# Kernel tuning notes

Hardware: AMD Instinct MI355X
Metric: run time of the kernel (lower is better)

The kernel has to match this reference:

```python
import jax, jax.numpy as jnp
import numpy as np

N = 4096
FEAT = 5
H = 128
L = 3
K = 4
HD = H // K  # 32


def setup_inputs() -> dict:
    key = jax.random.key(0)
    ks = jax.random.split(key, 24)
    node_features = jax.random.normal(ks[0], (N, FEAT), dtype=jnp.float32)
    u = jax.random.uniform(ks[1], (N, N), dtype=jnp.float32)
    adj = jnp.where(u < 0.01, u, 0.0)
    adj = adj / (adj.sum(axis=1, keepdims=True) + 1e-8)  # row-normalised
    mask = jax.random.randint(ks[2], (N,), 0, 2).astype(bool)
    s = 0.05
    return {
        'node_features': node_features,
        'adj': adj,
        'mask': mask,
        'Wi': jax.random.normal(ks[3], (FEAT, H), jnp.float32) * s,
        'bi': jnp.zeros((H,), jnp.float32),
        'gat_W': jax.random.normal(ks[4], (L, K, H, HD), jnp.float32) * s,
        'gat_a': jax.random.normal(ks[5], (L, K, 2 * HD), jnp.float32) * s,
        'ln_g': jnp.ones((L, H), jnp.float32),
        'ln_b': jnp.zeros((L, H), jnp.float32),
        'pW1': jax.random.normal(ks[6], (H, H // 2), jnp.float32) * s,
        'pb1': jnp.zeros((H // 2,), jnp.float32),
        'pW2': jax.random.normal(ks[7], (H // 2, 1), jnp.float32) * s,
        'pb2': jnp.zeros((1,), jnp.float32),
        'poolW': jax.random.normal(ks[8], (H, H), jnp.float32) * s,
        'poolb': jnp.zeros((H,), jnp.float32),
        'poolv': jax.random.normal(ks[9], (H,), jnp.float32) * s,
        'vW1': jax.random.normal(ks[10], (H, H // 2), jnp.float32) * s,
        'vb1': jnp.zeros((H // 2,), jnp.float32),
        'vW2': jax.random.normal(ks[11], (H // 2, 1), jnp.float32) * s,
        'vb2': jnp.zeros((1,), jnp.float32),
    }


def _layernorm(x, g, b, eps=1e-5):
    mu = x.mean(-1, keepdims=True)
    var = ((x - mu) ** 2).mean(-1, keepdims=True)
    return (x - mu) / jnp.sqrt(var + eps) * g + b


def reference(node_features, adj, mask, Wi, bi, gat_W, gat_a, ln_g, ln_b,
              pW1, pb1, pW2, pb2, poolW, poolb, poolv, vW1, vb1, vW2, vb2):
    n = node_features.shape[0]
    x = jax.nn.relu(node_features @ Wi + bi)  # (N, H)
    edge_mask = (adj > 0) | jnp.eye(n, dtype=bool)  # (N, N) incl self-loops
    n_layers = gat_W.shape[0]
    for l in range(n_layers):
        Wx = jnp.einsum('nd,kdh->knh', x, gat_W[l])  # (K, N, hd)
        a_src = jnp.einsum('knh,kh->kn', Wx, gat_a[l][:, :HD])  # (K, N)
        a_dst = jnp.einsum('knh,kh->kn', Wx, gat_a[l][:, HD:])  # (K, N)
        e = jax.nn.leaky_relu(a_src[:, :, None] + a_dst[:, None, :], 0.2)  # (K,N,N)
        e = jnp.where(edge_mask[None], e, -jnp.inf)
        alpha = jax.nn.softmax(e, axis=-1)  # softmax over neighbours j
        h = jax.nn.elu(jnp.einsum('kij,kjh->kih', alpha, Wx))  # (K, N, hd)
        out = jnp.transpose(h, (1, 0, 2)).reshape(n, -1)  # concat heads -> (N, H)
        out = out + x  # residual (Identity: in_dim == out_dim)
        x = _layernorm(out, ln_g[l], ln_b[l])
    # policy head
    logits = (jax.nn.relu(x @ pW1 + pb1) @ pW2 + pb2).squeeze(-1)  # (N,)
    logits = jnp.where(mask, logits, -jnp.inf)
    # attention pooling restricted to masked (valid) nodes
    scores = jnp.tanh(x @ poolW + poolb) @ poolv  # (N,)
    scores = jnp.where(mask, scores, -jnp.inf)
    beta = jax.nn.softmax(scores)
    pooled = (beta[:, None] * x).sum(0)  # (H,)
    value = (jax.nn.relu(pooled @ vW1 + vb1) @ vW2 + vb2).squeeze(-1)  # scalar
    return logits, value
```

## Files before the change

kernel.cpp:

```cpp
#include <hip/hip_runtime.h>

#define NN 4096
#define FEAT 5
#define H 128
#define HD 32
#define KH 4
#define NEG_INF (-__builtin_inff())
#define MASK_SENTINEL (-1e30f)

#define WS_FLAG  0
#define WS_DEG   256
#define WS_NBR   (WS_DEG + NN*4)
#define WS_X     (WS_NBR + NN*128*2)
#define WS_WX    (WS_X + NN*H*4)
#define WS_ATS   (WS_WX + KH*NN*HD*4)
#define WS_ATD   (WS_ATS + NN*16)
#define WS_PART  (WS_ATD + NN*16)
#define WS_ZPART (WS_PART + 256*H*4)

__device__ __forceinline__ float red64(float v) {
#pragma unroll
    for (int off = 32; off; off >>= 1) v += __shfl_xor(v, off, 64);
    return v;
}
__device__ __forceinline__ float red32(float v) {
#pragma unroll
    for (int off = 16; off; off >>= 1) v += __shfl_xor(v, off, 32);
    return v;
}
__device__ __forceinline__ float red32max(float v) {
#pragma unroll
    for (int off = 16; off; off >>= 1) v = fmaxf(v, __shfl_xor(v, off, 32));
    return v;
}
__device__ __forceinline__ bool read_mask(const void* mp, int f, int n) {
    if (f == 3) return ((const long long*)mp)[n] != 0;
    if (f == 1) return ((const int*)mp)[n] != 0;
    if (f == 2) return ((const float*)mp)[n] != 0.f;
    return ((const unsigned char*)mp)[n] != 0;
}

__global__ __launch_bounds__(256) void k_proj(
    const float* __restrict__ nf, const float* __restrict__ Wi,
    const float* __restrict__ bi, const void* mask, int* flag,
    float* __restrict__ xbuf) {
    int w = threadIdx.x >> 6, lane = threadIdx.x & 63;
    int n = blockIdx.x * 4 + w;
    float a1 = bi[lane], a2 = bi[64 + lane];
#pragma unroll
    for (int f = 0; f < FEAT; f++) {
        float xv = nf[n * FEAT + f];
        a1 += xv * Wi[f * H + lane];
        a2 += xv * Wi[f * H + 64 + lane];
    }
    xbuf[(size_t)n * H + lane] = fmaxf(a1, 0.f);
    xbuf[(size_t)n * H + 64 + lane] = fmaxf(a2, 0.f);
    if (blockIdx.x == 0 && w == 0) {
        const unsigned* ip = (const unsigned*)mask;
        const float* fp = (const float*)mask;
        bool i32ok = true, i64ok = true, f32ok = true;
        for (int i = lane; i < 1024; i += 64) {
            unsigned v = ip[i];
            if (v > 1u) i32ok = false;
            if (i & 1) { if (v != 0u) i64ok = false; }
            else       { if (v > 1u) i64ok = false; }
            float fv = fp[i];
            if (fv != 0.f && fv != 1.f) f32ok = false;
        }
        i32ok = (__ballot((int)i32ok) == ~0ull);
        i64ok = (__ballot((int)i64ok) == ~0ull);
        f32ok = (__ballot((int)f32ok) == ~0ull);
        if (lane == 0) *flag = i64ok ? 3 : (i32ok ? 1 : (f32ok ? 2 : 0));
    }
}

__global__ __launch_bounds__(256) void k_csr(
    const float* __restrict__ adj, int* __restrict__ deg,
    unsigned short* __restrict__ nbr) {
    __shared__ int ln[4][128];
    int w = threadIdx.x >> 6, lane = threadIdx.x & 63;
    int row = blockIdx.x * 4 + w;
    ln[w][lane] = 0; ln[w][64 + lane] = 0;
    const float4* arow = (const float4*)(adj + (size_t)row * NN);
    int cnt = 0;
    bool self = false;
    for (int c0 = 0; c0 < NN / 4; c0 += 64) {
        float4 v = arow[c0 + lane];
        int cb = (c0 + lane) * 4;
        float vals[4] = {v.x, v.y, v.z, v.w};
#pragma unroll
        for (int s = 0; s < 4; s++) {
            bool nz = vals[s] > 0.f;
            if (nz && cb + s == row) self = true;
            unsigned long long b = __ballot((int)nz);
            if (nz) {
                int pos = cnt + __popcll(b & ((1ull << lane) - 1ull));
                if (pos < 128) ln[w][pos] = cb + s;
            }
            cnt += __popcll(b);
        }
    }
    bool anyself = __any((int)self);
    if (!anyself) {
        if (lane == 0 && cnt < 128) ln[w][cnt] = row;
        cnt++;
    }
    int d = cnt < 128 ? cnt : 128;
    if (lane == 0) deg[row] = d;
    nbr[(size_t)row * 128 + lane] = (unsigned short)ln[w][lane];
    nbr[(size_t)row * 128 + 64 + lane] = (unsigned short)ln[w][64 + lane];
}

__global__ __launch_bounds__(256) void k_wx(
    const float* __restrict__ xbuf, const float* __restrict__ gw,
    const float* __restrict__ ga, float* __restrict__ Wx,
    float* __restrict__ attS, float* __restrict__ attD) {
    __shared__ float xs[8][H];
    int t = threadIdx.x;
    int k = t >> 6, lane = t & 63, dh = lane >> 5, h = lane & 31;
    int n0 = blockIdx.x * 8;
    ((float4*)xs)[t] = ((const float4*)(xbuf + (size_t)n0 * H))[t];
    __syncthreads();
    float acc[8] = {0, 0, 0, 0, 0, 0, 0, 0};
    const float* g = gw + (size_t)k * (H * HD) + h;
    for (int dd = 0; dd < 64; dd += 4) {
        int d = dh * 64 + dd;
        float w0 = g[(size_t)(d + 0) * HD];
        float w1 = g[(size_t)(d + 1) * HD];
        float w2 = g[(size_t)(d + 2) * HD];
        float w3 = g[(size_t)(d + 3) * HD];
#pragma unroll
        for (int nn = 0; nn < 8; nn++) {
            float4 xv = *(const float4*)&xs[nn][d];
            acc[nn] += xv.x * w0 + xv.y * w1 + xv.z * w2 + xv.w * w3;
        }
    }
    float aws = ga[k * 64 + h], awd = ga[k * 64 + 32 + h];
#pragma unroll
    for (int nn = 0; nn < 8; nn++) {
        float full = acc[nn] + __shfl_xor(acc[nn], 32, 64);
        float s = red32(full * aws);
        float dv = red32(full * awd);
        int n = n0 + nn;
        if (dh == 0) Wx[(size_t)k * NN * HD + (size_t)n * HD + h] = full;
        if (lane == 0) { attS[n * 4 + k] = s; attD[n * 4 + k] = dv; }
    }
}

__global__ __launch_bounds__(256) void k_agg(
    const int* __restrict__ degG, const unsigned short* __restrict__ nbrG,
    const float* __restrict__ Wx, const float4* __restrict__ attS4,
    const float4* __restrict__ attD4, const float* __restrict__ lng,
    const float* __restrict__ lnb, float* __restrict__ xbuf) {
    __shared__ int lds_nbr[4][128];
    __shared__ float lds_al[4][2][128];
    __shared__ float lds_red[2][2][2];
    int t = threadIdx.x, w = t >> 6, lane = t & 63;
    int nn = w >> 1, wp = w & 1;
    int node = blockIdx.x * 2 + nn;
    int hs = lane >> 5, h = lane & 31;
    int k = 2 * wp + hs;
    int d = degG[node];
    {
        const unsigned short* np = nbrG + (size_t)node * 128;
        ushort2 a = *(const ushort2*)(np + lane * 2);
        lds_nbr[w][lane * 2] = a.x;
        lds_nbr[w][lane * 2 + 1] = a.y;
    }
    float4 aSv = attS4[node];
    float ai = wp ? (hs ? aSv.w : aSv.z) : (hs ? aSv.y : aSv.x);
    float e[4];
#pragma unroll
    for (int r = 0; r < 4; r++) {
        int c = r * 32 + h;
        if (c < d) {
            float4 dv4 = attD4[lds_nbr[w][c]];
            float dvv = wp ? (hs ? dv4.w : dv4.z) : (hs ? dv4.y : dv4.x);
            float v = ai + dvv;
            e[r] = v > 0.f ? v : 0.2f * v;
        } else e[r] = NEG_INF;
    }
    float m = red32max(fmaxf(fmaxf(e[0], e[1]), fmaxf(e[2], e[3])));
    float p[4], s = 0.f;
#pragma unroll
    for (int r = 0; r < 4; r++) {
        p[r] = (r * 32 + h < d) ? __expf(e[r] - m) : 0.f;
        s += p[r];
    }
    s = red32(s);
    float inv = 1.f / s;
#pragma unroll
    for (int r = 0; r < 4; r++) lds_al[w][hs][r * 32 + h] = p[r] * inv;
    float acc = 0.f;
    const float* wxk = Wx + (size_t)k * NN * HD + h;
    const float* ap = lds_al[w][hs];
    const int* np2 = lds_nbr[w];
    int dpad = (d + 7) & ~7;
    for (int c0 = 0; c0 < dpad; c0 += 8) {
        float a0 = ap[c0], a1 = ap[c0+1], a2 = ap[c0+2], a3 = ap[c0+3];
        float a4 = ap[c0+4], a5 = ap[c0+5], a6 = ap[c0+6], a7 = ap[c0+7];
        int s0 = np2[c0], s1 = np2[c0+1], s2 = np2[c0+2], s3 = np2[c0+3];
        int s4 = np2[c0+4], s5 = np2[c0+5], s6 = np2[c0+6], s7 = np2[c0+7];
        float v0 = wxk[(size_t)s0 * HD], v1 = wxk[(size_t)s1 * HD];
        float v2 = wxk[(size_t)s2 * HD], v3 = wxk[(size_t)s3 * HD];
        float v4 = wxk[(size_t)s4 * HD], v5 = wxk[(size_t)s5 * HD];
        float v6 = wxk[(size_t)s6 * HD], v7 = wxk[(size_t)s7 * HD];
        acc += a0*v0 + a1*v1 + a2*v2 + a3*v3 + a4*v4 + a5*v5 + a6*v6 + a7*v7;
    }
    float hv = acc > 0.f ? acc : __expf(acc) - 1.f;
    int dim = wp * 64 + lane;
    float o = hv + xbuf[(size_t)node * H + dim];
    float ps = red64(o);
    if (lane == 0) lds_red[nn][wp][0] = ps;
    __syncthreads();
    float mu = (lds_red[nn][0][0] + lds_red[nn][1][0]) * (1.f / H);
    float dv = o - mu;
    float vs = red64(dv * dv);
    if (lane == 0) lds_red[nn][wp][1] = vs;
    __syncthreads();
    float var = (lds_red[nn][0][1] + lds_red[nn][1][1]) * (1.f / H);
    float rstd = rsqrtf(var + 1e-5f);
    xbuf[(size_t)node * H + dim] = dv * rstd * lng[dim] + lnb[dim];
}

__global__ __launch_bounds__(256) void k_heads(
    const float* __restrict__ xbuf, const float* __restrict__ pW1,
    const float* __restrict__ pb1, const float* __restrict__ pW2,
    const float* __restrict__ pb2, const float* __restrict__ poolW,
    const float* __restrict__ poolb, const float* __restrict__ poolv,
    const void* mask, const int* __restrict__ flag, float* __restrict__ out,
    float* __restrict__ part, float* __restrict__ zpart) {
    __shared__ float lds_x[16][H];
    __shared__ float lds_part[4][H];
    __shared__ float lds_z[4];
    int t = threadIdx.x, w = t >> 6, lane = t & 63;
    int n0b = blockIdx.x * 16;
    for (int idx = t; idx < 16 * H; idx += 256)
        lds_x[idx >> 7][idx & 127] = xbuf[(size_t)(n0b + (idx >> 7)) * H + (idx & 127)];
    __syncthreads();
    int nb = n0b + w * 4;
    float accp[4] = {0, 0, 0, 0}, acs1[4] = {0, 0, 0, 0}, acs2[4] = {0, 0, 0, 0};
#pragma unroll 2
    for (int d = 0; d < H; d++) {
        float w1 = pW1[d * 64 + lane];
        float q1 = poolW[d * H + lane];
        float q2 = poolW[d * H + 64 + lane];
#pragma unroll
        for (int nn = 0; nn < 4; nn++) {
            float xv = lds_x[w * 4 + nn][d];
            accp[nn] += xv * w1;
            acs1[nn] += xv * q1;
            acs2[nn] += xv * q2;
        }
    }
    int flg = *flag;
    float T = fminf(red64(fabsf(poolv[lane]) + fabsf(poolv[64 + lane])), 30.f);
    float pb1v = pb1[lane], pw2v = pW2[lane], pb2v = pb2[0];
    float pob1 = poolb[lane], pob2 = poolb[64 + lane];
    float pov1 = poolv[lane], pov2 = poolv[64 + lane];
    float pp1 = 0.f, pp2 = 0.f, zacc = 0.f;
#pragma unroll
    for (int nn = 0; nn < 4; nn++) {
        int node = nb + nn;
        float hp = red64(fmaxf(accp[nn] + pb1v, 0.f) * pw2v);
        float sc = red64(tanhf(acs1[nn] + pob1) * pov1 + tanhf(acs2[nn] + pob2) * pov2);
        bool mk = read_mask(mask, flg, node);
        if (lane == 0) out[node] = mk ? (hp + pb2v) : MASK_SENTINEL;
        float wn = mk ? __expf(sc - T) : 0.f;
        pp1 += wn * lds_x[w * 4 + nn][lane];
        pp2 += wn * lds_x[w * 4 + nn][64 + lane];
        zacc += wn;
    }
    lds_part[w][lane] = pp1;
    lds_part[w][64 + lane] = pp2;
    if (lane == 0) lds_z[w] = zacc;
    __syncthreads();
    if (w == 0) {
        float s1 = lds_part[0][lane] + lds_part[1][lane] + lds_part[2][lane] + lds_part[3][lane];
        float s2 = lds_part[0][64 + lane] + lds_part[1][64 + lane] +
                   lds_part[2][64 + lane] + lds_part[3][64 + lane];
        part[blockIdx.x * H + lane] = s1;
        part[blockIdx.x * H + 64 + lane] = s2;
        if (lane == 0) zpart[blockIdx.x] = lds_z[0] + lds_z[1] + lds_z[2] + lds_z[3];
    }
}

__global__ __launch_bounds__(256) void k_value(
    const float* __restrict__ part, const float* __restrict__ zpart,
    const float* __restrict__ vW1, const float* __restrict__ vb1,
    const float* __restrict__ vW2, const float* __restrict__ vb2,
    float* __restrict__ out) {
    __shared__ float fin[2][H];
    __shared__ float zfin[256];
    __shared__ float pooled[H];
    int t = threadIdx.x;
    int dim = t & 127, hb = t >> 7;
    float s = 0.f;
    for (int b = hb * 128; b < hb * 128 + 128; b++) s += part[b * H + dim];
    fin[hb][dim] = s;
    zfin[t] = zpart[t];
    __syncthreads();
    for (int off = 128; off; off >>= 1) {
        if (t < off) zfin[t] += zfin[t + off];
        __syncthreads();
    }
    float Z = zfin[0];
    if (t < H) pooled[t] = (fin[0][t] + fin[1][t]) / Z;
    __syncthreads();
    if (t < 64) {
        float acc = vb1[t];
        for (int d = 0; d < H; d++) acc += pooled[d] * vW1[d * 64 + t];
        float v = red64(fmaxf(acc, 0.f) * vW2[t]);
        if (t == 0) out[NN] = v + vb2[0];
    }
}

extern "C" void kernel_launch(void* const* d_in, const int* in_sizes, int n_in,
                              void* d_out, int out_size, void* d_ws, size_t ws_size,
                              hipStream_t stream) {
    const float* nf    = (const float*)d_in[0];
    const float* adj   = (const float*)d_in[1];
    const void*  mask  = d_in[2];
    const float* Wi    = (const float*)d_in[3];
    const float* bi    = (const float*)d_in[4];
    const float* gat_W = (const float*)d_in[5];
    const float* gat_a = (const float*)d_in[6];
    const float* ln_g  = (const float*)d_in[7];
    const float* ln_b  = (const float*)d_in[8];
    const float* pW1   = (const float*)d_in[9];
    const float* pb1   = (const float*)d_in[10];
    const float* pW2   = (const float*)d_in[11];
    const float* pb2   = (const float*)d_in[12];
    const float* poolW = (const float*)d_in[13];
    const float* poolb = (const float*)d_in[14];
    const float* poolv = (const float*)d_in[15];
    const float* vW1   = (const float*)d_in[16];
    const float* vb1   = (const float*)d_in[17];
    const float* vW2   = (const float*)d_in[18];
    const float* vb2   = (const float*)d_in[19];

    char* ws = (char*)d_ws;
    int*            flag = (int*)(ws + WS_FLAG);
    int*            deg  = (int*)(ws + WS_DEG);
    unsigned short* nbr  = (unsigned short*)(ws + WS_NBR);
    float* xbuf  = (float*)(ws + WS_X);
    float* Wx    = (float*)(ws + WS_WX);
    float* ats   = (float*)(ws + WS_ATS);
    float* atd   = (float*)(ws + WS_ATD);
    float* partb = (float*)(ws + WS_PART);
    float* zpart = (float*)(ws + WS_ZPART);
    float* out   = (float*)d_out;

    const size_t GWL = KH * H * HD;
    const size_t GAL = KH * 2 * HD;

    k_proj<<<1024, 256, 0, stream>>>(nf, Wi, bi, mask, flag, xbuf);
    k_csr<<<1024, 256, 0, stream>>>(adj, deg, nbr);
    for (int l = 0; l < 3; l++) {
        k_wx<<<512, 256, 0, stream>>>(xbuf, gat_W + l * GWL, gat_a + l * GAL,
                                      Wx, ats, atd);
        k_agg<<<2048, 256, 0, stream>>>(deg, nbr, Wx, (const float4*)ats,
                                        (const float4*)atd, ln_g + l * H,
                                        ln_b + l * H, xbuf);
    }
    k_heads<<<256, 256, 0, stream>>>(xbuf, pW1, pb1, pW2, pb2, poolW, poolb, poolv,
                                     mask, flag, out, partb, zpart);
    k_value<<<1, 256, 0, stream>>>(partb, zpart, vW1, vb1, vW2, vb2, out);
}
```

Baseline: 169.1 us.

## Spread GAT aggregation across 8 waves per node and shrink wx tile

k_agg now assigns one node per 512-thread block. Each head's neighbour range is split across two waves, and each half-wave gathers an interleaved subset of neighbours. Partial sums are combined through shared memory before the ELU, residual and layernorm. k_wx processes 4 nodes per block instead of 8, doubling its grid. The aim is more parallelism and latency hiding for the irregular gathers, at the cost of more block barriers, idle waves during the epilogue, and less weight reuse in k_wx.

Measured after the change: 192.8 us. 1.14x slower.

```diff
diff --git a/kernel.cpp b/kernel.cpp
--- a/kernel.cpp
+++ b/kernel.cpp
@@ -23,14 +23,14 @@
     for (int off = 32; off; off >>= 1) v += __shfl_xor(v, off, 64);
     return v;
 }
+__device__ __forceinline__ float red64max(float v) {
+#pragma unroll
+    for (int off = 32; off; off >>= 1) v = fmaxf(v, __shfl_xor(v, off, 64));
+    return v;
+}
 __device__ __forceinline__ float red32(float v) {
 #pragma unroll
     for (int off = 16; off; off >>= 1) v += __shfl_xor(v, off, 32);
-    return v;
-}
-__device__ __forceinline__ float red32max(float v) {
-#pragma unroll
-    for (int off = 16; off; off >>= 1) v = fmaxf(v, __shfl_xor(v, off, 32));
     return v;
 }
 __device__ __forceinline__ bool read_mask(const void* mp, int f, int n) {
@@ -115,13 +115,13 @@
     const float* __restrict__ xbuf, const float* __restrict__ gw,
     const float* __restrict__ ga, float* __restrict__ Wx,
     float* __restrict__ attS, float* __restrict__ attD) {
-    __shared__ float xs[8][H];
+    __shared__ float xs[4][H];
     int t = threadIdx.x;
     int k = t >> 6, lane = t & 63, dh = lane >> 5, h = lane & 31;
-    int n0 = blockIdx.x * 8;
-    ((float4*)xs)[t] = ((const float4*)(xbuf + (size_t)n0 * H))[t];
-    __syncthreads();
-    float acc[8] = {0, 0, 0, 0, 0, 0, 0, 0};
+    int n0 = blockIdx.x * 4;
+    if (t < 128) ((float4*)xs)[t] = ((const float4*)(xbuf + (size_t)n0 * H))[t];
+    __syncthreads();
+    float acc[4] = {0, 0, 0, 0};
     const float* g = gw + (size_t)k * (H * HD) + h;
     for (int dd = 0; dd < 64; dd += 4) {
         int d = dh * 64 + dd;
@@ -130,14 +130,14 @@
         float w2 = g[(size_t)(d + 2) * HD];
         float w3 = g[(size_t)(d + 3) * HD];
 #pragma unroll
-        for (int nn = 0; nn < 8; nn++) {
+        for (int nn = 0; nn < 4; nn++) {
             float4 xv = *(const float4*)&xs[nn][d];
             acc[nn] += xv.x * w0 + xv.y * w1 + xv.z * w2 + xv.w * w3;
         }
     }
     float aws = ga[k * 64 + h], awd = ga[k * 64 + 32 + h];
 #pragma unroll
-    for (int nn = 0; nn < 8; nn++) {
+    for (int nn = 0; nn < 4; nn++) {
         float full = acc[nn] + __shfl_xor(acc[nn], 32, 64);
         float s = red32(full * aws);
         float dv = red32(full * awd);
@@ -147,80 +147,90 @@
     }
 }
 
-__global__ __launch_bounds__(256) void k_agg(
+__global__ __launch_bounds__(512) void k_agg(
     const int* __restrict__ degG, const unsigned short* __restrict__ nbrG,
     const float* __restrict__ Wx, const float4* __restrict__ attS4,
     const float4* __restrict__ attD4, const float* __restrict__ lng,
     const float* __restrict__ lnb, float* __restrict__ xbuf) {
-    __shared__ int lds_nbr[4][128];
-    __shared__ float lds_al[4][2][128];
-    __shared__ float lds_red[2][2][2];
+    __shared__ int   s_nbr[132];
+    __shared__ float s_al[4][132];
+    __shared__ float s_m[4][2], s_s[4][2];
+    __shared__ float s_pacc[4][32];
+    __shared__ float s_red[4], s_red2[4];
     int t = threadIdx.x, w = t >> 6, lane = t & 63;
-    int nn = w >> 1, wp = w & 1;
-    int node = blockIdx.x * 2 + nn;
-    int hs = lane >> 5, h = lane & 31;
-    int k = 2 * wp + hs;
+    int node = blockIdx.x;
+    int k = w & 3, cs = w >> 2;
     int d = degG[node];
-    {
-        const unsigned short* np = nbrG + (size_t)node * 128;
-        ushort2 a = *(const ushort2*)(np + lane * 2);
-        lds_nbr[w][lane * 2] = a.x;
-        lds_nbr[w][lane * 2 + 1] = a.y;
-    }
+    if (t < 128) s_nbr[t] = nbrG[(size_t)node * 128 + t];
+    if (t < 4) s_nbr[128 + t] = 0;
+    if (w == 7 && lane < 16) s_al[lane & 3][128 + (lane >> 2)] = 0.f;
+    __syncthreads();
+    int c_e = cs * 64 + lane;
     float4 aSv = attS4[node];
-    float ai = wp ? (hs ? aSv.w : aSv.z) : (hs ? aSv.y : aSv.x);
-    float e[4];
-#pragma unroll
-    for (int r = 0; r < 4; r++) {
-        int c = r * 32 + h;
-        if (c < d) {
-            float4 dv4 = attD4[lds_nbr[w][c]];
-            float dvv = wp ? (hs ? dv4.w : dv4.z) : (hs ? dv4.y : dv4.x);
-            float v = ai + dvv;
-            e[r] = v > 0.f ? v : 0.2f * v;
-        } else e[r] = NEG_INF;
-    }
-    float m = red32max(fmaxf(fmaxf(e[0], e[1]), fmaxf(e[2], e[3])));
-    float p[4], s = 0.f;
-#pragma unroll
-    for (int r = 0; r < 4; r++) {
-        p[r] = (r * 32 + h < d) ? __expf(e[r] - m) : 0.f;
-        s += p[r];
-    }
-    s = red32(s);
-    float inv = 1.f / s;
-#pragma unroll
-    for (int r = 0; r < 4; r++) lds_al[w][hs][r * 32 + h] = p[r] * inv;
+    float ai = k == 0 ? aSv.x : k == 1 ? aSv.y : k == 2 ? aSv.z : aSv.w;
+    float e;
+    if (c_e < d) {
+        float4 dv4 = attD4[s_nbr[c_e]];
+        float dvv = k == 0 ? dv4.x : k == 1 ? dv4.y : k == 2 ? dv4.z : dv4.w;
+        float v = ai + dvv;
+        e = v > 0.f ? v : 0.2f * v;
+    } else e = NEG_INF;
+    float mh = red64max(e);
+    if (lane == 0) s_m[k][cs] = mh;
+    __syncthreads();
+    float mg = fmaxf(s_m[k][0], s_m[k][1]);
+    float p = (c_e < d) ? __expf(e - mg) : 0.f;
+    s_al[k][c_e] = p;
+    float sh = red64(p);
+    if (lane == 0) s_s[k][cs] = sh;
+    __syncthreads();
+    float inv = 1.f / (s_s[k][0] + s_s[k][1]);
+    int h = lane & 31, q = lane >> 5;
     float acc = 0.f;
     const float* wxk = Wx + (size_t)k * NN * HD + h;
-    const float* ap = lds_al[w][hs];
-    const int* np2 = lds_nbr[w];
-    int dpad = (d + 7) & ~7;
-    for (int c0 = 0; c0 < dpad; c0 += 8) {
-        float a0 = ap[c0], a1 = ap[c0+1], a2 = ap[c0+2], a3 = ap[c0+3];
-        float a4 = ap[c0+4], a5 = ap[c0+5], a6 = ap[c0+6], a7 = ap[c0+7];
-        int s0 = np2[c0], s1 = np2[c0+1], s2 = np2[c0+2], s3 = np2[c0+3];
-        int s4 = np2[c0+4], s5 = np2[c0+5], s6 = np2[c0+6], s7 = np2[c0+7];
-        float v0 = wxk[(size_t)s0 * HD], v1 = wxk[(size_t)s1 * HD];
-        float v2 = wxk[(size_t)s2 * HD], v3 = wxk[(size_t)s3 * HD];
-        float v4 = wxk[(size_t)s4 * HD], v5 = wxk[(size_t)s5 * HD];
-        float v6 = wxk[(size_t)s6 * HD], v7 = wxk[(size_t)s7 * HD];
-        acc += a0*v0 + a1*v1 + a2*v2 + a3*v3 + a4*v4 + a5*v5 + a6*v6 + a7*v7;
-    }
-    float hv = acc > 0.f ? acc : __expf(acc) - 1.f;
-    int dim = wp * 64 + lane;
-    float o = hv + xbuf[(size_t)node * H + dim];
-    float ps = red64(o);
-    if (lane == 0) lds_red[nn][wp][0] = ps;
-    __syncthreads();
-    float mu = (lds_red[nn][0][0] + lds_red[nn][1][0]) * (1.f / H);
+    int jmax = (d + 3) >> 2;
+    int cb = 2 * cs + q;
+    int j = 0;
+    for (; j + 4 <= jmax; j += 4) {
+        int c0 = j * 4 + cb, c1 = c0 + 4, c2 = c0 + 8, c3 = c0 + 12;
+        float a0 = s_al[k][c0], a1 = s_al[k][c1], a2 = s_al[k][c2], a3 = s_al[k][c3];
+        int n0 = s_nbr[c0], n1 = s_nbr[c1], n2 = s_nbr[c2], n3 = s_nbr[c3];
+        float v0 = wxk[(size_t)n0 * HD], v1 = wxk[(size_t)n1 * HD];
+        float v2 = wxk[(size_t)n2 * HD], v3 = wxk[(size_t)n3 * HD];
+        acc += a0 * v0 + a1 * v1 + a2 * v2 + a3 * v3;
+    }
+    for (; j < jmax; j++) {
+        int c0 = j * 4 + cb;
+        acc += s_al[k][c0] * wxk[(size_t)s_nbr[c0] * HD];
+    }
+    acc *= inv;
+    acc += __shfl_xor(acc, 32, 64);
+    if (cs == 1 && lane < 32) s_pacc[k][h] = acc;
+    __syncthreads();
+    float o = 0.f;
+    if (cs == 0 && lane < 32) {
+        float tot = acc + s_pacc[k][h];
+        float hv = tot > 0.f ? tot : __expf(tot) - 1.f;
+        o = hv + xbuf[(size_t)node * H + k * 32 + h];
+    }
+    if (cs == 0) {
+        float r = red32(o);
+        if (lane == 0) s_red[k] = r;
+    }
+    __syncthreads();
+    float mu = (s_red[0] + s_red[1] + s_red[2] + s_red[3]) * (1.f / H);
     float dv = o - mu;
-    float vs = red64(dv * dv);
-    if (lane == 0) lds_red[nn][wp][1] = vs;
-    __syncthreads();
-    float var = (lds_red[nn][0][1] + lds_red[nn][1][1]) * (1.f / H);
-    float rstd = rsqrtf(var + 1e-5f);
-    xbuf[(size_t)node * H + dim] = dv * rstd * lng[dim] + lnb[dim];
+    if (cs == 0) {
+        float vs = red32(lane < 32 ? dv * dv : 0.f);
+        if (lane == 0) s_red2[k] = vs;
+    }
+    __syncthreads();
+    if (cs == 0 && lane < 32) {
+        float var = (s_red2[0] + s_red2[1] + s_red2[2] + s_red2[3]) * (1.f / H);
+        float rstd = rsqrtf(var + 1e-5f);
+        int dim = k * 32 + h;
+        xbuf[(size_t)node * H + dim] = dv * rstd * lng[dim] + lnb[dim];
+    }
 }
 
 __global__ __launch_bounds__(256) void k_heads(
@@ -357,9 +367,9 @@
     k_proj<<<1024, 256, 0, stream>>>(nf, Wi, bi, mask, flag, xbuf);
     k_csr<<<1024, 256, 0, stream>>>(adj, deg, nbr);
     for (int l = 0; l < 3; l++) {
-        k_wx<<<512, 256, 0, stream>>>(xbuf, gat_W + l * GWL, gat_a + l * GAL,
-                                      Wx, ats, atd);
-        k_agg<<<2048, 256, 0, stream>>>(deg, nbr, Wx, (const float4*)ats,
+        k_wx<<<1024, 256, 0, stream>>>(xbuf, gat_W + l * GWL, gat_a + l * GAL,
+                                       Wx, ats, atd);
+        k_agg<<<4096, 512, 0, stream>>>(deg, nbr, Wx, (const float4*)ats,
                                         (const float4*)atd, ln_g + l * H,
                                         ln_b + l * H, xbuf);
     }
```
